# Performance work log

Hardware: AMD Instinct MI355X
Metric: run time of the kernel (lower is better)

The kernel has to match this reference:

```python
import jax, jax.numpy as jnp
import numpy as np

EMBED_DIM = 1024
NUM_HEADS = 16
HEAD_DIM = EMBED_DIM // NUM_HEADS
B, S = 4, 2048


def setup_inputs() -> dict:
    key = jax.random.key(0)
    ks = jax.random.split(key, 9)
    scale = 1.0 / np.sqrt(EMBED_DIM)
    x = jax.random.normal(ks[0], (B, S, EMBED_DIM), dtype=jnp.float32)
    # nn.Linear weights are [out, in]; we store as [in, out] for x @ W
    Wq = jax.random.uniform(ks[1], (EMBED_DIM, EMBED_DIM), jnp.float32, -scale, scale)
    bq = jax.random.uniform(ks[2], (EMBED_DIM,), jnp.float32, -scale, scale)
    Wk = jax.random.uniform(ks[3], (EMBED_DIM, EMBED_DIM), jnp.float32, -scale, scale)
    bk = jax.random.uniform(ks[4], (EMBED_DIM,), jnp.float32, -scale, scale)
    Wv = jax.random.uniform(ks[5], (EMBED_DIM, EMBED_DIM), jnp.float32, -scale, scale)
    bv = jax.random.uniform(ks[6], (EMBED_DIM,), jnp.float32, -scale, scale)
    Wo = jax.random.uniform(ks[7], (EMBED_DIM, EMBED_DIM), jnp.float32, -scale, scale)
    bo = jax.random.uniform(ks[8], (EMBED_DIM,), jnp.float32, -scale, scale)
    return {"x": x, "Wq": Wq, "bq": bq, "Wk": Wk, "bk": bk,
            "Wv": Wv, "bv": bv, "Wo": Wo, "bo": bo}


def reference(x, Wq, bq, Wk, bk, Wv, bv, Wo, bo):
    Bsz, Slen, E = x.shape
    H, D = NUM_HEADS, HEAD_DIM
    # projections -> [B, H, S, D]
    def split_heads(t):
        return t.reshape(Bsz, Slen, H, D).transpose(0, 2, 1, 3)
    q = split_heads(x @ Wq + bq)
    k = split_heads(x @ Wk + bk)
    v = split_heads(x @ Wv + bv)
    # scores [B, H, S, S]
    scores = jnp.einsum('bhqd,bhkd->bhqk', q, k) / jnp.sqrt(jnp.float32(D))
    attn = jax.nn.softmax(scores, axis=-1)  # dropout p=0.0 -> identity
    out = jnp.einsum('bhqk,bhkd->bhqd', attn, v)  # [B, H, S, D]
    out = out.transpose(0, 2, 1, 3).reshape(Bsz, Slen, E)
    return out @ Wo + bo
```

## Files before the change

### kernel.cpp

```cpp
#include <hip/hip_runtime.h>

typedef __bf16 bf16x8 __attribute__((ext_vector_type(8)));
typedef float floatx4 __attribute__((ext_vector_type(4)));

#define B_   4
#define H_   16
#define S_   2048
#define D_   64
#define E_   1024
#define BS_  8192

#define QSCALE 0.18033688011112042f

__device__ __forceinline__ floatx4 mfma16(bf16x8 a, bf16x8 b, floatx4 c) {
  return __builtin_amdgcn_mfma_f32_16x16x32_bf16(a, b, c, 0, 0, 0);
}

__device__ __forceinline__ unsigned short f2bf(float f) {
  union { float f; unsigned int u; } a;
  a.f = f;
  unsigned int u = a.u;
  return (unsigned short)((u + 0x7fffu + ((u >> 16) & 1u)) >> 16);
}

__global__ __launch_bounds__(256) void transpose4(
    const float* __restrict__ W0, const float* __restrict__ W1,
    const float* __restrict__ W2, const float* __restrict__ W3,
    unsigned short* __restrict__ Wt) {
  __shared__ float tile[32][33];
  const float* src = blockIdx.z == 0 ? W0 : blockIdx.z == 1 ? W1
                   : blockIdx.z == 2 ? W2 : W3;
  unsigned short* dst = Wt + (size_t)blockIdx.z * E_ * E_;
  const int k0 = blockIdx.x * 32, n0 = blockIdx.y * 32;
  const int tx = threadIdx.x, ty = threadIdx.y;
#pragma unroll
  for (int i = 0; i < 32; i += 8)
    tile[ty + i][tx] = src[(size_t)(k0 + ty + i) * E_ + n0 + tx];
  __syncthreads();
#pragma unroll
  for (int i = 0; i < 32; i += 8)
    dst[(size_t)(n0 + ty + i) * E_ + k0 + tx] = f2bf(tile[tx][ty + i]);
}

__global__ __launch_bounds__(256) void cast_x(
    const float* __restrict__ x, unsigned short* __restrict__ xb) {
  const size_t i = ((size_t)blockIdx.x * 256 + threadIdx.x) * 8;
  const float4* p = (const float4*)(x + i);
  float4 a0 = p[0], a1 = p[1];
  union { unsigned short h[8]; uint4 u; } pk;
  pk.h[0] = f2bf(a0.x); pk.h[1] = f2bf(a0.y); pk.h[2] = f2bf(a0.z); pk.h[3] = f2bf(a0.w);
  pk.h[4] = f2bf(a1.x); pk.h[5] = f2bf(a1.y); pk.h[6] = f2bf(a1.z); pk.h[7] = f2bf(a1.w);
  *(uint4*)(xb + i) = pk.u;
}

__global__ __launch_bounds__(256) void gemm_qkv(
    const unsigned short* __restrict__ xb, const unsigned short* __restrict__ Wt,
    const float* __restrict__ bq, const float* __restrict__ bk,
    const float* __restrict__ bv,
    unsigned short* __restrict__ Q, unsigned short* __restrict__ K,
    unsigned short* __restrict__ V) {
  __shared__ __align__(16) unsigned short As[128][40];
  __shared__ __align__(16) unsigned short Bs[128][40];
  const int t = threadIdx.x;
  const int w = t >> 6, lane = t & 63, quad = lane >> 4, l15 = lane & 15;
  const int moff = (w >> 1) * 64, noff = (w & 1) * 64;
  const int m0 = blockIdx.y * 128, n0 = blockIdx.x * 128;
  const int srow = t >> 1;
  const int scol = (t & 1) * 16;

  floatx4 acc[4][4] = {};

  for (int k0 = 0; k0 < E_; k0 += 32) {
    const uint4* ap = (const uint4*)(xb + (size_t)(m0 + srow) * E_ + k0 + scol);
    uint4 a0 = ap[0], a1 = ap[1];
    *(uint4*)&As[srow][scol]     = a0;
    *(uint4*)&As[srow][scol + 8] = a1;
    const uint4* bp = (const uint4*)(Wt + (size_t)(n0 + srow) * E_ + k0 + scol);
    uint4 b0 = bp[0], b1 = bp[1];
    *(uint4*)&Bs[srow][scol]     = b0;
    *(uint4*)&Bs[srow][scol + 8] = b1;
    __syncthreads();

    bf16x8 af[4], bf[4];
#pragma unroll
    for (int i = 0; i < 4; i++) af[i] = *(const bf16x8*)&As[moff + i * 16 + l15][quad * 8];
#pragma unroll
    for (int j = 0; j < 4; j++) bf[j] = *(const bf16x8*)&Bs[noff + j * 16 + l15][quad * 8];
#pragma unroll
    for (int i = 0; i < 4; i++)
#pragma unroll
      for (int j = 0; j < 4; j++) acc[i][j] = mfma16(af[i], bf[j], acc[i][j]);
    __syncthreads();
  }

  const int which = n0 >> 10;
  const float* bias = which == 0 ? bq : (which == 1 ? bk : bv);
  unsigned short* dst = which == 0 ? Q : (which == 1 ? K : V);
  const float sc = which == 0 ? QSCALE : 1.0f;
#pragma unroll
  for (int j = 0; j < 4; j++) {
    const int n = (n0 + noff + j * 16 + l15) & 1023;
    const int h = n >> 6, d = n & 63;
    const float bb = bias[n];
#pragma unroll
    for (int i = 0; i < 4; i++) {
#pragma unroll
      for (int r = 0; r < 4; r++) {
        const int m = m0 + moff + i * 16 + quad * 4 + r;
        const int b = m >> 11, s = m & 2047;
        const float val = (acc[i][j][r] + bb) * sc;
        if (which == 2)
          dst[(((size_t)(b * H_ + h) * D_) + d) * S_ + s] = f2bf(val);
        else
          dst[(((size_t)(b * H_ + h) * S_) + s) * D_ + d] = f2bf(val);
      }
    }
  }
}

__global__ __launch_bounds__(256, 4) void attn_kernel(
    const unsigned short* __restrict__ Q, const unsigned short* __restrict__ K,
    const unsigned short* __restrict__ Vt, unsigned short* __restrict__ AO) {
  __shared__ __align__(16) unsigned short Ks[64][72];
  __shared__ __align__(16) unsigned short Vs[64][72];
  __shared__ __align__(16) unsigned short Ps[128][76];
  const int t = threadIdx.x;
  const int w = t >> 6, lane = t & 63, quad = lane >> 4, l15 = lane & 15;
  const int bh = blockIdx.y;
  const int q0 = blockIdx.x * 128;
  const int qb = w * 32;
  const size_t base = (size_t)bh * S_ * D_;

  bf16x8 qf[2][2];
#pragma unroll
  for (int mt = 0; mt < 2; mt++)
#pragma unroll
    for (int ks = 0; ks < 2; ks++)
      qf[mt][ks] = *(const bf16x8*)(Q + base +
                    (size_t)(q0 + qb + mt * 16 + l15) * D_ + ks * 32 + quad * 8);

  float l_i[2][4] = {};
  floatx4 O[2][4] = {};

  const int kk = t >> 2, cc = (t & 3) * 16;
  const unsigned short* kp = K  + base + (size_t)kk * D_ + cc;
  const unsigned short* vp = Vt + base + (size_t)kk * S_ + cc;

  uint4 kr0 = *(const uint4*)(kp);
  uint4 kr1 = *(const uint4*)(kp + 8);
  uint4 vr0 = *(const uint4*)(vp);
  uint4 vr1 = *(const uint4*)(vp + 8);

  for (int kt0 = 0; kt0 < S_; kt0 += 64) {
    *(uint4*)&Ks[kk][cc]     = kr0;
    *(uint4*)&Ks[kk][cc + 8] = kr1;
    *(uint4*)&Vs[kk][cc]     = vr0;
    *(uint4*)&Vs[kk][cc + 8] = vr1;
    __syncthreads();

    if (kt0 + 64 < S_) {
      kr0 = *(const uint4*)(kp + (size_t)(kt0 + 64) * D_);
      kr1 = *(const uint4*)(kp + (size_t)(kt0 + 64) * D_ + 8);
      vr0 = *(const uint4*)(vp + kt0 + 64);
      vr1 = *(const uint4*)(vp + kt0 + 72);
    }

    floatx4 s[2][4] = {};
#pragma unroll
    for (int kt = 0; kt < 4; kt++) {
#pragma unroll
      for (int ks = 0; ks < 2; ks++) {
        bf16x8 kf = *(const bf16x8*)&Ks[kt * 16 + l15][ks * 32 + quad * 8];
#pragma unroll
        for (int mt = 0; mt < 2; mt++) s[mt][kt] = mfma16(qf[mt][ks], kf, s[mt][kt]);
      }
    }

#pragma unroll
    for (int mt = 0; mt < 2; mt++) {
#pragma unroll
      for (int kt = 0; kt < 4; kt++) {
#pragma unroll
        for (int r = 0; r < 4; r++) {
          const float pv = __builtin_amdgcn_exp2f(s[mt][kt][r]);
          l_i[mt][r] += pv;
          Ps[qb + mt * 16 + quad * 4 + r][kt * 16 + l15] = f2bf(pv);
        }
      }
    }

#pragma unroll
    for (int ks = 0; ks < 2; ks++) {
      bf16x8 pf[2];
#pragma unroll
      for (int mt = 0; mt < 2; mt++)
        pf[mt] = *(const bf16x8*)&Ps[qb + mt * 16 + l15][ks * 32 + quad * 8];
#pragma unroll
      for (int dt = 0; dt < 4; dt++) {
        bf16x8 vf = *(const bf16x8*)&Vs[dt * 16 + l15][ks * 32 + quad * 8];
#pragma unroll
        for (int mt = 0; mt < 2; mt++) O[mt][dt] = mfma16(pf[mt], vf, O[mt][dt]);
      }
    }
    __syncthreads();
  }

  const int b = bh >> 4, h = bh & 15;
#pragma unroll
  for (int mt = 0; mt < 2; mt++)
#pragma unroll
    for (int r = 0; r < 4; r++) {
      float sum = l_i[mt][r];
#pragma unroll
      for (int off = 1; off < 16; off <<= 1) sum += __shfl_xor(sum, off, 64);
      const float inv = 1.f / sum;
      const int srow = q0 + qb + mt * 16 + quad * 4 + r;
      unsigned short* aop = AO + (size_t)(b * S_ + srow) * E_ + h * D_ + l15;
#pragma unroll
      for (int dt = 0; dt < 4; dt++)
        aop[dt * 16] = f2bf(O[mt][dt][r] * inv);
    }
}

__global__ __launch_bounds__(256) void gemm_out(
    const unsigned short* __restrict__ A, const unsigned short* __restrict__ Wt,
    const float* __restrict__ bo, float* __restrict__ Cout) {
  __shared__ __align__(16) unsigned short As[128][40];
  __shared__ __align__(16) unsigned short Bs[128][40];
  const int t = threadIdx.x;
  const int w = t >> 6, lane = t & 63, quad = lane >> 4, l15 = lane & 15;
  const int moff = (w >> 1) * 64, noff = (w & 1) * 64;
  const int m0 = blockIdx.y * 128, n0 = blockIdx.x * 128;
  const int srow = t >> 1;
  const int scol = (t & 1) * 16;

  floatx4 acc[4][4] = {};

  for (int k0 = 0; k0 < E_; k0 += 32) {
    const uint4* ap = (const uint4*)(A + (size_t)(m0 + srow) * E_ + k0 + scol);
    uint4 a0 = ap[0], a1 = ap[1];
    *(uint4*)&As[srow][scol]     = a0;
    *(uint4*)&As[srow][scol + 8] = a1;
    const uint4* bp = (const uint4*)(Wt + (size_t)(n0 + srow) * E_ + k0 + scol);
    uint4 b0 = bp[0], b1 = bp[1];
    *(uint4*)&Bs[srow][scol]     = b0;
    *(uint4*)&Bs[srow][scol + 8] = b1;
    __syncthreads();

    bf16x8 af[4], bf[4];
#pragma unroll
    for (int i = 0; i < 4; i++) af[i] = *(const bf16x8*)&As[moff + i * 16 + l15][quad * 8];
#pragma unroll
    for (int j = 0; j < 4; j++) bf[j] = *(const bf16x8*)&Bs[noff + j * 16 + l15][quad * 8];
#pragma unroll
    for (int i = 0; i < 4; i++)
#pragma unroll
      for (int j = 0; j < 4; j++) acc[i][j] = mfma16(af[i], bf[j], acc[i][j]);
    __syncthreads();
  }

#pragma unroll
  for (int j = 0; j < 4; j++) {
    const int n = n0 + noff + j * 16 + l15;
    const float bb = bo[n];
#pragma unroll
    for (int i = 0; i < 4; i++) {
#pragma unroll
      for (int r = 0; r < 4; r++) {
        const int m = m0 + moff + i * 16 + quad * 4 + r;
        Cout[(size_t)m * E_ + n] = acc[i][j][r] + bb;
      }
    }
  }
}

extern "C" void kernel_launch(void* const* d_in, const int* in_sizes, int n_in,
                              void* d_out, int out_size, void* d_ws, size_t ws_size,
                              hipStream_t stream) {
  const float* x  = (const float*)d_in[0];
  const float* Wq = (const float*)d_in[1];
  const float* bq = (const float*)d_in[2];
  const float* Wk = (const float*)d_in[3];
  const float* bk = (const float*)d_in[4];
  const float* Wv = (const float*)d_in[5];
  const float* bv = (const float*)d_in[6];
  const float* Wo = (const float*)d_in[7];
  const float* bo = (const float*)d_in[8];
  float* out = (float*)d_out;

  unsigned short* Wt = (unsigned short*)d_ws;
  unsigned short* Qb = Wt + (size_t)4 * E_ * E_;
  unsigned short* Kb = Qb + (size_t)B_ * H_ * S_ * D_;
  unsigned short* Vb = Kb + (size_t)B_ * H_ * S_ * D_;
  unsigned short* xb = Vb + (size_t)B_ * H_ * S_ * D_;
  unsigned short* AO = xb;

  transpose4<<<dim3(32, 32, 4), dim3(32, 8), 0, stream>>>(Wq, Wk, Wv, Wo, Wt);
  cast_x<<<dim3(BS_ * E_ / (256 * 8)), 256, 0, stream>>>(x, xb);
  gemm_qkv<<<dim3(24, 64), 256, 0, stream>>>(xb, Wt, bq, bk, bv, Qb, Kb, Vb);
  attn_kernel<<<dim3(16, 64), 256, 0, stream>>>(Qb, Kb, Vb, AO);
  gemm_out<<<dim3(8, 64), 256, 0, stream>>>(AO, Wt + (size_t)3 * E_ * E_, bo, out);
}
```

Before: 347.2 us.

## Use direct global-to-LDS async loads with XOR-swizzled tiles in projection GEMMs

```diff
diff --git a/kernel.cpp b/kernel.cpp
--- a/kernel.cpp
+++ b/kernel.cpp
@@ -21,6 +21,12 @@
   a.f = f;
   unsigned int u = a.u;
   return (unsigned short)((u + 0x7fffu + ((u >> 16) & 1u)) >> 16);
+}
+
+__device__ __forceinline__ void async16(const unsigned short* g, unsigned short* l) {
+  __builtin_amdgcn_global_load_lds(
+      (const __attribute__((address_space(1))) unsigned int*)g,
+      (__attribute__((address_space(3))) unsigned int*)l, 16, 0, 0);
 }
 
 __global__ __launch_bounds__(256) void transpose4(
@@ -53,45 +59,55 @@
   *(uint4*)(xb + i) = pk.u;
 }
 
+#define GEMM_CORE(APTR, BPTR)                                                  \
+  __shared__ __align__(16) unsigned short As[128][32];                         \
+  __shared__ __align__(16) unsigned short Bs[128][32];                         \
+  const int t = threadIdx.x;                                                   \
+  const int w = t >> 6, lane = t & 63, quad = lane >> 4, l15 = lane & 15;      \
+  const int moff = (w >> 1) * 64, noff = (w & 1) * 64;                         \
+  const int m0 = blockIdx.y * 128, n0 = blockIdx.x * 128;                      \
+  const int r_loc = lane >> 2, cphys = lane & 3;                               \
+  const int r0 = w * 32 + r_loc, r1 = r0 + 16;                                 \
+  const int sw = (r0 & 3) ^ ((r0 >> 2) & 1);         \
+  const int clog = (cphys ^ sw) * 8;                                           \
+  const unsigned short* gA0 = (APTR) + (size_t)(m0 + r0) * E_ + clog;          \
+  const unsigned short* gA1 = (APTR) + (size_t)(m0 + r1) * E_ + clog;          \
+  const unsigned short* gB0 = (BPTR) + (size_t)(n0 + r0) * E_ + clog;          \
+  const unsigned short* gB1 = (BPTR) + (size_t)(n0 + r1) * E_ + clog;          \
+  unsigned short* lA0 = &As[w * 32][0];                                        \
+  unsigned short* lA1 = &As[w * 32 + 16][0];                                   \
+  unsigned short* lB0 = &Bs[w * 32][0];                                        \
+  unsigned short* lB1 = &Bs[w * 32 + 16][0];                                   \
+  const int sF = (l15 & 3) ^ ((l15 >> 2) & 1);          \
+  const int fcol = ((quad ^ sF)) * 8;                                          \
+  floatx4 acc[4][4] = {};                                                      \
+  for (int k0 = 0; k0 < E_; k0 += 32) {                                        \
+    async16(gA0 + k0, lA0);                                                    \
+    async16(gA1 + k0, lA1);                                                    \
+    async16(gB0 + k0, lB0);                                                    \
+    async16(gB1 + k0, lB1);                                                    \
+    __syncthreads();                     \
+    bf16x8 af[4], bf[4];                                                       \
+    _Pragma("unroll")                                                          \
+    for (int i = 0; i < 4; i++)                                                \
+      af[i] = *(const bf16x8*)&As[moff + i * 16 + l15][fcol];                  \
+    _Pragma("unroll")                                                          \
+    for (int j = 0; j < 4; j++)                                                \
+      bf[j] = *(const bf16x8*)&Bs[noff + j * 16 + l15][fcol];                  \
+    _Pragma("unroll")                                                          \
+    for (int i = 0; i < 4; i++)                                                \
+      _Pragma("unroll")                                                        \
+      for (int j = 0; j < 4; j++) acc[i][j] = mfma16(af[i], bf[j], acc[i][j]); \
+    __syncthreads();                              \
+  }
+
 __global__ __launch_bounds__(256) void gemm_qkv(
     const unsigned short* __restrict__ xb, const unsigned short* __restrict__ Wt,
     const float* __restrict__ bq, const float* __restrict__ bk,
     const float* __restrict__ bv,
     unsigned short* __restrict__ Q, unsigned short* __restrict__ K,
     unsigned short* __restrict__ V) {
-  __shared__ __align__(16) unsigned short As[128][40];
-  __shared__ __align__(16) unsigned short Bs[128][40];
-  const int t = threadIdx.x;
-  const int w = t >> 6, lane = t & 63, quad = lane >> 4, l15 = lane & 15;
-  const int moff = (w >> 1) * 64, noff = (w & 1) * 64;
-  const int m0 = blockIdx.y * 128, n0 = blockIdx.x * 128;
-  const int srow = t >> 1;
-  const int scol = (t & 1) * 16;
-
-  floatx4 acc[4][4] = {};
-
-  for (int k0 = 0; k0 < E_; k0 += 32) {
-    const uint4* ap = (const uint4*)(xb + (size_t)(m0 + srow) * E_ + k0 + scol);
-    uint4 a0 = ap[0], a1 = ap[1];
-    *(uint4*)&As[srow][scol]     = a0;
-    *(uint4*)&As[srow][scol + 8] = a1;
-    const uint4* bp = (const uint4*)(Wt + (size_t)(n0 + srow) * E_ + k0 + scol);
-    uint4 b0 = bp[0], b1 = bp[1];
-    *(uint4*)&Bs[srow][scol]     = b0;
-    *(uint4*)&Bs[srow][scol + 8] = b1;
-    __syncthreads();
-
-    bf16x8 af[4], bf[4];
-#pragma unroll
-    for (int i = 0; i < 4; i++) af[i] = *(const bf16x8*)&As[moff + i * 16 + l15][quad * 8];
-#pragma unroll
-    for (int j = 0; j < 4; j++) bf[j] = *(const bf16x8*)&Bs[noff + j * 16 + l15][quad * 8];
-#pragma unroll
-    for (int i = 0; i < 4; i++)
-#pragma unroll
-      for (int j = 0; j < 4; j++) acc[i][j] = mfma16(af[i], bf[j], acc[i][j]);
-    __syncthreads();
-  }
+  GEMM_CORE(xb, Wt)
 
   const int which = n0 >> 10;
   const float* bias = which == 0 ? bq : (which == 1 ? bk : bv);
@@ -225,39 +241,7 @@
 __global__ __launch_bounds__(256) void gemm_out(
     const unsigned short* __restrict__ A, const unsigned short* __restrict__ Wt,
     const float* __restrict__ bo, float* __restrict__ Cout) {
-  __shared__ __align__(16) unsigned short As[128][40];
-  __shared__ __align__(16) unsigned short Bs[128][40];
-  const int t = threadIdx.x;
-  const int w = t >> 6, lane = t & 63, quad = lane >> 4, l15 = lane & 15;
-  const int moff = (w >> 1) * 64, noff = (w & 1) * 64;
-  const int m0 = blockIdx.y * 128, n0 = blockIdx.x * 128;
-  const int srow = t >> 1;
-  const int scol = (t & 1) * 16;
-
-  floatx4 acc[4][4] = {};
-
-  for (int k0 = 0; k0 < E_; k0 += 32) {
-    const uint4* ap = (const uint4*)(A + (size_t)(m0 + srow) * E_ + k0 + scol);
-    uint4 a0 = ap[0], a1 = ap[1];
-    *(uint4*)&As[srow][scol]     = a0;
-    *(uint4*)&As[srow][scol + 8] = a1;
-    const uint4* bp = (const uint4*)(Wt + (size_t)(n0 + srow) * E_ + k0 + scol);
-    uint4 b0 = bp[0], b1 = bp[1];
-    *(uint4*)&Bs[srow][scol]     = b0;
-    *(uint4*)&Bs[srow][scol + 8] = b1;
-    __syncthreads();
-
-    bf16x8 af[4], bf[4];
-#pragma unroll
-    for (int i = 0; i < 4; i++) af[i] = *(const bf16x8*)&As[moff + i * 16 + l15][quad * 8];
-#pragma unroll
-    for (int j = 0; j < 4; j++) bf[j] = *(const bf16x8*)&Bs[noff + j * 16 + l15][quad * 8];
-#pragma unroll
-    for (int i = 0; i < 4; i++)
-#pragma unroll
-      for (int j = 0; j < 4; j++) acc[i][j] = mfma16(af[i], bf[j], acc[i][j]);
-    __syncthreads();
-  }
+  GEMM_CORE(A, Wt)
 
 #pragma unroll
   for (int j = 0; j < 4; j++) {
```

Result: faster. 314.7 us (-9.3%).
